# Kernel optimization log

Hardware: AMD Instinct MI355X
Metric: run time of the kernel (lower is better)

The kernel has to match this reference:

```python
import jax, jax.numpy as jnp
import numpy as np

B, N, F, U = 16, 2048, 64, 64

def setup_inputs() -> dict:
    key = jax.random.key(0)
    k1, k2, k3 = jax.random.split(key, 3)
    node_features = jax.random.normal(k1, (B, N, F), dtype=jnp.float32)
    adjacency_matrix = (jax.random.uniform(k2, (B, N, N)) < 0.01).astype(jnp.float32)
    kernel = jax.random.normal(k3, (F, U), dtype=jnp.float32) * (1.0 / np.sqrt(F))
    return {"node_features": node_features, "adjacency_matrix": adjacency_matrix, "kernel": kernel}

def reference(node_features, adjacency_matrix, kernel):
    # A_tilde = A + I  (self-loops)
    n = adjacency_matrix.shape[-1]
    adj = adjacency_matrix + jnp.eye(n, dtype=adjacency_matrix.dtype)
    # symmetric normalization D^-1/2 A_tilde D^-1/2 (diag matmuls == broadcast scaling)
    row_sum = jnp.sum(adj, axis=-1)                      # [B, N]
    d_inv_sqrt = jnp.where(row_sum > 0, row_sum ** -0.5, 0.0)
    norm_adj = d_inv_sqrt[:, :, None] * adj * d_inv_sqrt[:, None, :]
    # feature transform then aggregate, fused with ReLU
    transformed = jnp.einsum('bnf,fu->bnu', node_features, kernel)
    out = jnp.einsum('bnm,bmu->bnu', norm_adj, transformed)
    return jax.nn.relu(out)
```

## Files before the change

kernel.cpp:

```cpp
#include <hip/hip_runtime.h>
#include <hip/hip_bf16.h>


#define NB     16
#define NN     2048
#define NF     64
#define NU     64
#define NROWS  (NB * NN)
#define NGRP   (NROWS / 4)

typedef float vfloat4 __attribute__((ext_vector_type(4)));
typedef unsigned int uint;
typedef uint vuint4 __attribute__((ext_vector_type(4)));

__device__ __forceinline__ int map_row(int g, int wid) {
    const int x = g & 7, s = g >> 3;
    const int batch = x + ((s >> 9) << 3);
    const int grp = s & 511;
    return (batch << 11) + (grp << 2) + wid;
}

__global__ __launch_bounds__(256) void k1_rowsum_compact(
    const float* __restrict__ A, float* __restrict__ d,
    int* __restrict__ counts, int* __restrict__ idx, int cap)
{
    const int t = threadIdx.x, wid = t >> 6, lane = t & 63;
    const int row = map_row(blockIdx.x, wid);
    const uint* Arow = reinterpret_cast<const uint*>(A + (size_t)row * NN);
    const unsigned long long lmask_lt = (lane == 63) ? 0x7fffffffffffffffull
                                                     : ((1ull << lane) - 1ull);
    vuint4 a[8];
    #pragma unroll
    for (int c = 0; c < 8; ++c)
        a[c] = __builtin_nontemporal_load(
            reinterpret_cast<const vuint4*>(Arow) + c * 64 + lane);

    const size_t base = (size_t)row * cap;
    int cnt = 0;
    #pragma unroll
    for (int c = 0; c < 8; ++c) {
        #pragma unroll
        for (int e = 0; e < 4; ++e) {
            const bool nz = (a[c][e] != 0u);
            const unsigned long long m = __ballot(nz);
            if (m) {
                if (nz) {
                    const int slot = cnt + __popcll(m & lmask_lt);
                    if (slot < cap)
                        idx[base + slot] = ((c * 64 + lane) << 2) + e;
                }
                cnt += __popcll(m);
            }
        }
    }
    if (lane == 0) {
        d[row]      = rsqrtf((float)cnt + 1.0f);
        counts[row] = cnt;
    }
}

__global__ __launch_bounds__(256) void k2_transform_scale(
    const float* __restrict__ X, const float* __restrict__ W,
    const float* __restrict__ d, float* __restrict__ Tp)
{
    __shared__ float sW[NF * NU];
    const int t = threadIdx.x, wid = t >> 6, lane = t & 63;
    #pragma unroll
    for (int k = 0; k < 4; ++k)
        reinterpret_cast<float4*>(sW)[t + 256 * k] =
            reinterpret_cast<const float4*>(W)[t + 256 * k];
    __syncthreads();

    const int row = map_row(blockIdx.x, wid);
    const float xv = X[(size_t)row * NF + lane];
    const float dr = d[row];
    float acc = 0.f;
    #pragma unroll
    for (int f = 0; f < NF; ++f)
        acc += __shfl(xv, f) * sW[f * NU + lane];
    Tp[(size_t)row * NU + lane] = acc * dr;
}

__global__ __launch_bounds__(256) void k3_aggregate(
    const float* __restrict__ A, const float* __restrict__ Tp,
    const float* __restrict__ d, const int* __restrict__ counts,
    const int* __restrict__ idx, float* __restrict__ out, int cap)
{
    const int t = threadIdx.x, wid = t >> 6, lane = t & 63;
    const int row = map_row(blockIdx.x, wid);
    const int b   = row >> 11;
    const float* Tb = Tp + (((size_t)b) << 11) * NU;

    float a0 = Tp[(size_t)row * NU + lane];
    float a1 = 0.f;
    const int cnt = counts[row];
    if (cnt <= cap) {
        const size_t base = (size_t)row * cap;
        const int4* q4 = reinterpret_cast<const int4*>(idx + base);
        const int nfull = cnt >> 2;
        for (int q = 0; q < nfull; ++q) {
            const int4 qq = q4[q];
            const float t0 = Tb[((size_t)(uint)qq.x << 6) + lane];
            const float t1 = Tb[((size_t)(uint)qq.y << 6) + lane];
            const float t2 = Tb[((size_t)(uint)qq.z << 6) + lane];
            const float t3 = Tb[((size_t)(uint)qq.w << 6) + lane];
            a0 += t0 + t2;
            a1 += t1 + t3;
        }
        for (int k = nfull << 2; k < cnt; ++k)
            a1 += Tb[((size_t)(uint)idx[base + k] << 6) + lane];
    } else {
        const float* Arow = A + (size_t)row * NN;
        for (int j = 0; j < NN; ++j)
            if (Arow[j] != 0.f) a1 += Tb[((size_t)j << 6) + lane];
    }
    const float r = d[row] * (a0 + a1);
    out[(size_t)row * NU + lane] = r > 0.f ? r : 0.f;
}

extern "C" void kernel_launch(void* const* d_in, const int* in_sizes, int n_in,
                              void* d_out, int out_size, void* d_ws, size_t ws_size,
                              hipStream_t stream)
{
    const float* X = (const float*)d_in[0];
    const float* A = (const float*)d_in[1];
    const float* W = (const float*)d_in[2];
    float* out = (float*)d_out;

    char* ws = (char*)d_ws;
    float* Tp     = (float*)ws;
    float* dvec   = (float*)(ws + (size_t)NROWS * NU * 4);
    int*   counts = (int*)  (ws + (size_t)NROWS * NU * 4 + (size_t)NROWS * 4);
    int*   idx    = (int*)  (ws + (size_t)NROWS * NU * 4 + 2ull * NROWS * 4);

    const size_t fixed = (size_t)NROWS * NU * 4 + 2ull * NROWS * 4;
    int cap = 0;
    if (ws_size > fixed) {
        size_t c = (ws_size - fixed) / ((size_t)NROWS * sizeof(int));
        cap = (int)(c < 128 ? c : 128);
        cap &= ~3;
    }

    k1_rowsum_compact<<<NGRP, 256, 0, stream>>>(A, dvec, counts, idx, cap);
    k2_transform_scale<<<NGRP, 256, 0, stream>>>(X, W, dvec, Tp);
    k3_aggregate<<<NGRP, 256, 0, stream>>>(A, Tp, dvec, counts, idx, out, cap);
}
```

Baseline: 396.1 us.

## Fuse adjacency scan and feature transform into one persistent-style kernel

Merges the row-sum/compaction kernel and the X·W transform kernel into a single kernel. Each block loops over several row groups, so the shared-memory weight load happens once per block rather than once per group. The matmul is placed between the adjacency loads and the ballot scan to hide memory latency. This removes one kernel launch and the round-trip of d through global memory, but cuts the grid size and may reduce the number of in-flight loads, which matters for the bandwidth-bound 256MB adjacency scan.

Result: slower. 420.3 us (+6.1%).

```diff
diff --git a/kernel.cpp b/kernel.cpp
--- a/kernel.cpp
+++ b/kernel.cpp
@@ -8,8 +8,9 @@
 #define NU     64
 #define NROWS  (NB * NN)
 #define NGRP   (NROWS / 4)
+#define NBLK   2048
+#define K12IT  (NGRP / NBLK)
 
-typedef float vfloat4 __attribute__((ext_vector_type(4)));
 typedef unsigned int uint;
 typedef uint vuint4 __attribute__((ext_vector_type(4)));
 
@@ -20,48 +21,11 @@
     return (batch << 11) + (grp << 2) + wid;
 }
 
-__global__ __launch_bounds__(256) void k1_rowsum_compact(
-    const float* __restrict__ A, float* __restrict__ d,
-    int* __restrict__ counts, int* __restrict__ idx, int cap)
-{
-    const int t = threadIdx.x, wid = t >> 6, lane = t & 63;
-    const int row = map_row(blockIdx.x, wid);
-    const uint* Arow = reinterpret_cast<const uint*>(A + (size_t)row * NN);
-    const unsigned long long lmask_lt = (lane == 63) ? 0x7fffffffffffffffull
-                                                     : ((1ull << lane) - 1ull);
-    vuint4 a[8];
-    #pragma unroll
-    for (int c = 0; c < 8; ++c)
-        a[c] = __builtin_nontemporal_load(
-            reinterpret_cast<const vuint4*>(Arow) + c * 64 + lane);
-
-    const size_t base = (size_t)row * cap;
-    int cnt = 0;
-    #pragma unroll
-    for (int c = 0; c < 8; ++c) {
-        #pragma unroll
-        for (int e = 0; e < 4; ++e) {
-            const bool nz = (a[c][e] != 0u);
-            const unsigned long long m = __ballot(nz);
-            if (m) {
-                if (nz) {
-                    const int slot = cnt + __popcll(m & lmask_lt);
-                    if (slot < cap)
-                        idx[base + slot] = ((c * 64 + lane) << 2) + e;
-                }
-                cnt += __popcll(m);
-            }
-        }
-    }
-    if (lane == 0) {
-        d[row]      = rsqrtf((float)cnt + 1.0f);
-        counts[row] = cnt;
-    }
-}
-
-__global__ __launch_bounds__(256) void k2_transform_scale(
-    const float* __restrict__ X, const float* __restrict__ W,
-    const float* __restrict__ d, float* __restrict__ Tp)
+__global__ __launch_bounds__(256) void k12_scan_transform(
+    const float* __restrict__ X, const float* __restrict__ A,
+    const float* __restrict__ W, float* __restrict__ Tp,
+    float* __restrict__ d, int* __restrict__ counts,
+    int* __restrict__ idx, int cap)
 {
     __shared__ float sW[NF * NU];
     const int t = threadIdx.x, wid = t >> 6, lane = t & 63;
@@ -71,14 +35,48 @@
             reinterpret_cast<const float4*>(W)[t + 256 * k];
     __syncthreads();
 
-    const int row = map_row(blockIdx.x, wid);
-    const float xv = X[(size_t)row * NF + lane];
-    const float dr = d[row];
-    float acc = 0.f;
-    #pragma unroll
-    for (int f = 0; f < NF; ++f)
-        acc += __shfl(xv, f) * sW[f * NU + lane];
-    Tp[(size_t)row * NU + lane] = acc * dr;
+    const unsigned long long lmask_lt = (lane == 63) ? 0x7fffffffffffffffull
+                                                     : ((1ull << lane) - 1ull);
+    for (int it = 0; it < K12IT; ++it) {
+        const int g   = blockIdx.x + it * NBLK;
+        const int row = map_row(g, wid);
+
+        const float xv = X[(size_t)row * NF + lane];
+        const uint* Arow = reinterpret_cast<const uint*>(A + (size_t)row * NN);
+        vuint4 a[8];
+        #pragma unroll
+        for (int c = 0; c < 8; ++c)
+            a[c] = __builtin_nontemporal_load(
+                reinterpret_cast<const vuint4*>(Arow) + c * 64 + lane);
+
+        float acc = 0.f;
+        #pragma unroll
+        for (int f = 0; f < NF; ++f)
+            acc += __shfl(xv, f) * sW[f * NU + lane];
+
+        const size_t base = (size_t)row * cap;
+        int cnt = 0;
+        #pragma unroll
+        for (int c = 0; c < 8; ++c) {
+            #pragma unroll
+            for (int e = 0; e < 4; ++e) {
+                const bool nz = (a[c][e] != 0u);
+                const unsigned long long m = __ballot(nz);
+                if (m) {
+                    if (nz) {
+                        const int slot = cnt + __popcll(m & lmask_lt);
+                        if (slot < cap)
+                            idx[base + slot] = ((c * 64 + lane) << 2) + e;
+                    }
+                    cnt += __popcll(m);
+                }
+            }
+        }
+
+        const float di = rsqrtf((float)cnt + 1.0f);
+        if (lane == 0) { d[row] = di; counts[row] = cnt; }
+        Tp[(size_t)row * NU + lane] = acc * di;
+    }
 }
 
 __global__ __launch_bounds__(256) void k3_aggregate(
@@ -141,7 +139,6 @@
         cap &= ~3;
     }
 
-    k1_rowsum_compact<<<NGRP, 256, 0, stream>>>(A, dvec, counts, idx, cap);
-    k2_transform_scale<<<NGRP, 256, 0, stream>>>(X, W, dvec, Tp);
+    k12_scan_transform<<<NBLK, 256, 0, stream>>>(X, A, W, Tp, dvec, counts, idx, cap);
     k3_aggregate<<<NGRP, 256, 0, stream>>>(A, Tp, dvec, counts, idx, out, cap);
 }
```
